# Optimization experiments

Measured on AMD Instinct MI355X. Metric: run time of the kernel, lower is better.

## Reference

```python
import jax, jax.numpy as jnp
import numpy as np
from jax.scipy.special import logsumexp

N_NODES = 10000
DEG = 16            # fixed out-degree -> 1-hop neighborhood size m = DEG + 1
N_TPL = 16
TPL_N = 10
N_FEAT = 128
N_SINK = 10         # Sinkhorn iterations for the linear OT subproblem
N_CG = 4            # Frank-Wolfe (conditional gradient) iterations for FGW


def setup_inputs() -> dict:
    key = jax.random.key(0)
    k1, k2, k3 = jax.random.split(key, 3)
    x = jax.random.normal(k1, (N_NODES, N_FEAT), jnp.float32)
    # structured fixed-degree graph: node i -> (i+1..i+DEG) mod N, sorted by source
    src = jnp.repeat(jnp.arange(N_NODES), DEG)
    dst = ((jnp.arange(N_NODES)[:, None] + jnp.arange(1, DEG + 1)[None, :]) % N_NODES).reshape(-1)
    edge_index = jnp.stack([src, dst])
    R = jax.random.uniform(k2, (N_TPL, TPL_N, TPL_N), jnp.float32)
    templates = 0.5 * (R + jnp.swapaxes(R, 1, 2))           # symmetric, as in template_initialisation
    templates_features = 0.001 * jax.random.normal(k3, (N_TPL, TPL_N, N_FEAT), jnp.float32)
    q0 = jnp.zeros((N_TPL, TPL_N), jnp.float32)
    alpha0 = jnp.zeros((1,), jnp.float32)
    return {"x": x, "templates": templates, "templates_features": templates_features,
            "q0": q0, "alpha0": alpha0, "edge_index": edge_index}


def _sinkhorn_log(G, logp, logq, reg):
    """Entropic OT plan for cost G [m,n], marginals exp(logp), exp(logq); log-domain."""
    def body(carry, _):
        f, g = carry
        f = reg * logp - reg * logsumexp((g[None, :] - G) / reg, axis=1)
        g = reg * logq - reg * logsumexp((f[:, None] - G) / reg, axis=0)
        return (f, g), None
    (f, g), _ = jax.lax.scan(jax.checkpoint(body),
                             (jnp.zeros_like(logp), jnp.zeros_like(logq)), None, length=N_SINK)
    return jnp.exp((f[:, None] + g[None, :] - G) / reg)


def _fgw(C1, F1, p, C2, F2, q, alpha):
    """Fused GW distance (square loss) between (C1 [m,m], F1 [m,d], p [m]) and
    (C2 [n,n], F2 [n,d], q [n]) via conditional gradient with Sinkhorn LP solver."""
    # squared-euclidean feature cost  [m,n]
    M = jnp.sum(F1 * F1, 1)[:, None] + jnp.sum(F2 * F2, 1)[None, :] - 2.0 * (F1 @ F2.T)
    # constant term of the square-loss GW tensor product
    constC = ((C1 * C1) @ p)[:, None] + ((C2 * C2) @ q)[None, :]
    logp, logq = jnp.log(p), jnp.log(q)
    T0 = p[:, None] * q[None, :]

    def cg(T, _):
        CTC = C1 @ T @ C2                                   # [m,n]
        Gr = (1.0 - alpha) * M + 2.0 * alpha * (constC - 2.0 * CTC)   # FGW gradient
        reg = 0.01 * jnp.max(jnp.abs(Gr)) + 1e-8            # small entropic reg ~ EMD
        Tn = _sinkhorn_log(Gr, logp, logq, reg)
        D = Tn - T
        CDC = C1 @ D @ C2
        # E(T + t D) is quadratic in t:  a t^2 + b t + const
        a = -2.0 * alpha * jnp.sum(CDC * D)
        b = (1.0 - alpha) * jnp.sum(M * D) + alpha * (jnp.sum(constC * D) - 4.0 * jnp.sum(CTC * D))
        t = jnp.where(a > 0, jnp.clip(-b / (2.0 * a + 1e-16), 0.0, 1.0),
                      jnp.where(a + b < 0, 1.0, 0.0))
        return T + t * D, None

    T, _ = jax.lax.scan(jax.checkpoint(cg), T0, None, length=N_CG)
    return (1.0 - alpha) * jnp.sum(M * T) + alpha * jnp.sum((constC - 2.0 * C1 @ T @ C2) * T)


def reference(x, templates, templates_features, q0, alpha0, edge_index):
    N, d = x.shape
    deg = edge_index.shape[1] // N
    m = deg + 1
    neighbors = edge_index[1].reshape(N, deg)                       # sorted-by-source
    local = jnp.concatenate([jnp.arange(N)[:, None], neighbors], 1)  # [N,m] node + 1-hop
    # local adjacency: edge (a,b) iff local[b] in neighbors(local[a]); symmetrized
    neigh_loc = neighbors[local]                                    # [N,m,deg]
    C1 = (neigh_loc[:, :, None, :] == local[:, None, :, None]).any(-1).astype(x.dtype)
    C1 = jnp.maximum(C1, jnp.swapaxes(C1, 1, 2))                    # [N,m,m]
    F1 = x[local]                                                   # [N,m,d]
    alpha = jax.nn.sigmoid(alpha0[0])
    q = jax.nn.softmax(q0, axis=1)                                  # [K,n]
    p = jnp.full((m,), 1.0 / m, x.dtype)
    over_tpl = jax.vmap(_fgw, in_axes=(None, None, None, 0, 0, 0, None))
    over_nodes = jax.vmap(over_tpl, in_axes=(0, 0, None, None, None, None, None))
    dist = over_nodes(C1, F1, p, templates, templates_features, q, alpha)  # [N,K]
    return jnp.log(dist)
```

## Files before the change

kernel.cpp:

```cpp
#include <hip/hip_runtime.h>
#include <math.h>

#define NN    10000
#define MM    17
#define KT    16
#define TN    10
#define NH    5
#define NF    128
#define NSINK 10
#define NCG   4
#define DOTLD (NN*TN)

typedef float v2f __attribute__((ext_vector_type(2)));
__device__ __forceinline__ v2f mk2(float x, float y) { v2f r; r.x = x; r.y = y; return r; }

#define ELEM(arr, b2) (((b2) & 1) ? arr[(b2) >> 1].y : arr[(b2) >> 1].x)

template <int CTRL>
__device__ __forceinline__ float dppf(float v) {
    return __int_as_float(__builtin_amdgcn_update_dpp(
        0, __float_as_int(v), CTRL, 0xF, 0xF, true));
}
__device__ __forceinline__ float rsum4(float v) {
    v += dppf<0xB1>(v);
    v += dppf<0x4E>(v);
    return v;
}
__device__ __forceinline__ float rmax4(float v) {
    v = fmaxf(v, dppf<0xB1>(v));
    v = fmaxf(v, dppf<0x4E>(v));
    return v;
}

__device__ __forceinline__ float dot4(float4 a, float4 b) {
    return a.x*b.x + a.y*b.y + a.z*b.z + a.w*b.w;
}

__global__ __launch_bounds__(256)
void precompute_kernel(const float* __restrict__ x, const float* __restrict__ tfeat,
                       float* __restrict__ dot_t, float* __restrict__ xnorm,
                       float* __restrict__ tfnorm)
{
    __shared__ float4 tfs[TN * (NF / 4)];
    __shared__ float4 xs[256 * 4];

    const int k   = blockIdx.y;
    const int v0  = blockIdx.x * 256;
    const int tid = threadIdx.x;
    const int v   = v0 + tid;
    const int vc  = (v < NN) ? v : (NN - 1);

    const float4* tf4 = (const float4*)(tfeat + (size_t)k * TN * NF);
    for (int u = tid; u < TN * (NF / 4); u += 256) tfs[u] = tf4[u];
    __syncthreads();

    if (blockIdx.x == 0 && tid < TN) {
        float s = 0.f;
        #pragma unroll 8
        for (int c = 0; c < NF / 4; ++c) { float4 u = tfs[tid * (NF / 4) + c]; s += dot4(u, u); }
        tfnorm[k * TN + tid] = s;
    }

    float acc[TN];
    #pragma unroll
    for (int j = 0; j < TN; ++j) acc[j] = 0.f;
    float xa = 0.f;

    const float4* x4 = (const float4*)x;
    for (int ch = 0; ch < 8; ++ch) {
        __syncthreads();
        for (int u = tid; u < 256 * 4; u += 256) {
            int vr = u >> 2, c4 = u & 3;
            int vv = v0 + vr; if (vv >= NN) vv = NN - 1;
            xs[u] = x4[(size_t)vv * (NF / 4) + ch * 4 + c4];
        }
        __syncthreads();
        float4 xv0 = xs[tid * 4 + 0], xv1 = xs[tid * 4 + 1],
               xv2 = xs[tid * 4 + 2], xv3 = xs[tid * 4 + 3];
        xa += dot4(xv0, xv0) + dot4(xv1, xv1) + dot4(xv2, xv2) + dot4(xv3, xv3);
        #pragma unroll
        for (int j = 0; j < TN; ++j) {
            const float4* tr = &tfs[j * (NF / 4) + ch * 4];
            acc[j] += dot4(xv0, tr[0]) + dot4(xv1, tr[1])
                    + dot4(xv2, tr[2]) + dot4(xv3, tr[3]);
        }
    }

    if (v < NN) {
        float* dst = dot_t + (size_t)k * DOTLD + (size_t)vc * TN;
        #pragma unroll
        for (int j = 0; j < NH; ++j) {
            *(v2f*)(dst + 2 * j) = mk2(acc[2 * j], acc[2 * j + 1]);
        }
        if (k == 0) xnorm[vc] = xa;
    }
}

__global__ __launch_bounds__(256, 2)
void fgw_main(const float* __restrict__ dot_t,
              const float* __restrict__ xnorm,
              const float* __restrict__ tfnorm,
              const float* __restrict__ templates,
              const float* __restrict__ q0,
              const float* __restrict__ alpha0,
              float* __restrict__ out)
{
    const int k    = blockIdx.y;
    const int tid  = threadIdx.x;
    const int l    = tid & 3;
    const int node = blockIdx.x * 64 + (tid >> 2);

    const float* __restrict__ C2  = templates + k * (TN * TN);
    const float* __restrict__ q0r = q0 + k * TN;
    const float* __restrict__ tfn = tfnorm + k * TN;
    const float* __restrict__ dk  = dot_t + (size_t)k * DOTLD;

    const float alpha = 1.0f / (1.0f + __expf(-alpha0[0]));
    const float oma   = 1.0f - alpha;
    const float t2a   = 2.0f * alpha;

    float qs_[TN];
    float qmax = q0r[0];
    #pragma unroll
    for (int b = 1; b < TN; ++b) qmax = fmaxf(qmax, q0r[b]);
    float qsum = 0.f;
    #pragma unroll
    for (int b = 0; b < TN; ++b) { qs_[b] = __expf(q0r[b] - qmax); qsum += qs_[b]; }
    float inv_qs = 1.0f / qsum;
    v2f qv2[NH];
    #pragma unroll
    for (int j = 0; j < NH; ++j) qv2[j] = mk2(qs_[2*j] * inv_qs, qs_[2*j+1] * inv_qs);

    v2f accc[NH], base[NH];
    #pragma unroll
    for (int j = 0; j < NH; ++j) { accc[j] = mk2(0.f, 0.f); base[j] = mk2(0.f, 0.f); }
    #pragma unroll
    for (int b2 = 0; b2 < TN; ++b2) {
        float qb2 = ELEM(qv2, b2);
        #pragma unroll
        for (int j = 0; j < NH; ++j) {
            v2f cr = mk2(C2[(2*j) * TN + b2], C2[(2*j+1) * TN + b2]);
            v2f cc = *(const v2f*)(C2 + b2 * TN + 2*j);
            accc[j] += (cr * cr) * qb2;
            base[j] += qb2 * cc;
        }
    }
    #pragma unroll
    for (int j = 0; j < NH; ++j) {
        accc[j] = alpha * (accc[j] + (float)(MM - 1) / (float)MM);
        base[j] = 2.0f * accc[j] - (4.0f * alpha * (float)(MM - 1) / (float)MM) * base[j];
    }

    int v1 = node + l;      if (v1 >= NN) v1 -= NN;
    int v2 = node + l + 4;  if (v2 >= NN) v2 -= NN;
    int v3 = node + l + 8;  if (v3 >= NN) v3 -= NN;
    int v4 = node + l + 12; if (v4 >= NN) v4 -= NN;
    int vB = node + 16;     if (vB >= NN) vB -= NN;
    const float ox1 = oma * xnorm[v1], ox2 = oma * xnorm[v2], ox3 = oma * xnorm[v3],
                ox4 = oma * xnorm[v4], oxB = oma * xnorm[vB];
    const float m2o = -2.0f * oma;
    const float* __restrict__ d1 = dk + (size_t)v1 * TN;
    const float* __restrict__ d2 = dk + (size_t)v2 * TN;
    const float* __restrict__ d3 = dk + (size_t)v3 * TN;
    const float* __restrict__ d4 = dk + (size_t)v4 * TN;
    const float* __restrict__ dB = dk + (size_t)vB * TN;

    v2f Gr1[NH], Gr2[NH], Gr3[NH], Gr4[NH], GrB[NH];
    #pragma unroll
    for (int j = 0; j < NH; ++j) {
        v2f bt = base[j] + oma * mk2(tfn[2*j], tfn[2*j+1]);
        Gr1[j] = (bt + ox1) + m2o * (*(const v2f*)(d1 + 2*j));
        Gr2[j] = (bt + ox2) + m2o * (*(const v2f*)(d2 + 2*j));
        Gr3[j] = (bt + ox3) + m2o * (*(const v2f*)(d3 + 2*j));
        Gr4[j] = (bt + ox4) + m2o * (*(const v2f*)(d4 + 2*j));
        GrB[j] = (bt + oxB) + m2o * (*(const v2f*)(dB + 2*j));
    }

    v2f T1[NH], T2[NH], T3[NH], T4[NH], TB[NH];
    #pragma unroll
    for (int j = 0; j < NH; ++j) {
        v2f t0 = (1.0f / (float)MM) * qv2[j];
        T1[j] = t0; T2[j] = t0; T3[j] = t0; T4[j] = t0; TB[j] = t0;
    }

    for (int cg = 0; cg < NCG; ++cg) {
        float gm = 0.f;
        #pragma unroll
        for (int j = 0; j < NH; ++j) {
            gm = fmaxf(gm, fmaxf(fabsf(Gr1[j].x), fabsf(Gr1[j].y)));
            gm = fmaxf(gm, fmaxf(fabsf(Gr2[j].x), fabsf(Gr2[j].y)));
            gm = fmaxf(gm, fmaxf(fabsf(Gr3[j].x), fabsf(Gr3[j].y)));
            gm = fmaxf(gm, fmaxf(fabsf(Gr4[j].x), fabsf(Gr4[j].y)));
            gm = fmaxf(gm, fmaxf(fabsf(GrB[j].x), fabsf(GrB[j].y)));
        }
        gm = rmax4(gm);
        const float reg = 0.01f * gm + 1e-8f;
        const float invreg = 1.0f / reg;

        float r1 = fminf(Gr1[0].x, Gr1[0].y), r2 = fminf(Gr2[0].x, Gr2[0].y);
        float r3 = fminf(Gr3[0].x, Gr3[0].y), r4 = fminf(Gr4[0].x, Gr4[0].y);
        float rB = fminf(GrB[0].x, GrB[0].y);
        #pragma unroll
        for (int j = 1; j < NH; ++j) {
            r1 = fminf(r1, fminf(Gr1[j].x, Gr1[j].y));
            r2 = fminf(r2, fminf(Gr2[j].x, Gr2[j].y));
            r3 = fminf(r3, fminf(Gr3[j].x, Gr3[j].y));
            r4 = fminf(r4, fminf(Gr4[j].x, Gr4[j].y));
            rB = fminf(rB, fminf(GrB[j].x, GrB[j].y));
        }
        v2f E1[NH], E2[NH], E3[NH], E4[NH], EB[NH];
        #pragma unroll
        for (int j = 0; j < NH; ++j) {
            v2f a1 = (r1 - Gr1[j]) * invreg; E1[j] = mk2(__expf(a1.x), __expf(a1.y));
            v2f a2 = (r2 - Gr2[j]) * invreg; E2[j] = mk2(__expf(a2.x), __expf(a2.y));
            v2f a3 = (r3 - Gr3[j]) * invreg; E3[j] = mk2(__expf(a3.x), __expf(a3.y));
            v2f a4 = (r4 - Gr4[j]) * invreg; E4[j] = mk2(__expf(a4.x), __expf(a4.y));
            v2f aB = (rB - GrB[j]) * invreg; EB[j] = mk2(__expf(aB.x), __expf(aB.y));
        }

        v2f egp[NH];
        #pragma unroll
        for (int j = 0; j < NH; ++j) egp[j] = mk2(1.f, 1.f);
        float w1 = 0.f, w2 = 0.f, w3 = 0.f, w4 = 0.f, wB = 0.f;
        for (int it = 0; it < NSINK; ++it) {
            v2f a1 = mk2(0.f,0.f), a2 = mk2(0.f,0.f), a3 = mk2(0.f,0.f),
                a4 = mk2(0.f,0.f), aB = mk2(0.f,0.f);
            #pragma unroll
            for (int j = 0; j < NH; ++j) {
                a1 += egp[j] * E1[j]; a2 += egp[j] * E2[j]; a3 += egp[j] * E3[j];
                a4 += egp[j] * E4[j]; aB += egp[j] * EB[j];
            }
            w1 = __builtin_amdgcn_rcpf(a1.x + a1.y);
            w2 = __builtin_amdgcn_rcpf(a2.x + a2.y);
            w3 = __builtin_amdgcn_rcpf(a3.x + a3.y);
            w4 = __builtin_amdgcn_rcpf(a4.x + a4.y);
            wB = __builtin_amdgcn_rcpf(aB.x + aB.y);
            #pragma unroll
            for (int j = 0; j < NH; ++j) {
                v2f t = w1 * E1[j] + w2 * E2[j] + w3 * E3[j] + w4 * E4[j];
                float Sx = fmaf(wB, EB[j].x, rsum4(t.x));
                float Sy = fmaf(wB, EB[j].y, rsum4(t.y));
                egp[j] = qv2[j] * mk2(__builtin_amdgcn_rcpf(Sx), __builtin_amdgcn_rcpf(Sy));
            }
        }

        v2f D1[NH], D2[NH], D3[NH], D4[NH], DB[NH];
        #pragma unroll
        for (int j = 0; j < NH; ++j) {
            D1[j] = (w1 * egp[j]) * E1[j] - T1[j];
            D2[j] = (w2 * egp[j]) * E2[j] - T2[j];
            D3[j] = (w3 * egp[j]) * E3[j] - T3[j];
            D4[j] = (w4 * egp[j]) * E4[j] - T4[j];
            DB[j] = (wB * egp[j]) * EB[j] - TB[j];
        }
        v2f cs[NH];
        #pragma unroll
        for (int j = 0; j < NH; ++j) {
            v2f dp = D1[j] + D2[j] + D3[j] + D4[j];
            cs[j] = mk2(rsum4(dp.x), rsum4(dp.y)) + DB[j];
        }
        v2f cdc1[NH], cdc2[NH], cdc3[NH], cdc4[NH], cdcB[NH];
        #pragma unroll
        for (int j = 0; j < NH; ++j) {
            cdc1[j] = mk2(0.f,0.f); cdc2[j] = mk2(0.f,0.f); cdc3[j] = mk2(0.f,0.f);
            cdc4[j] = mk2(0.f,0.f); cdcB[j] = mk2(0.f,0.f);
        }
        #pragma unroll
        for (int b2 = 0; b2 < TN; ++b2) {
            float csb = ELEM(cs, b2);
            float u1 = csb - ELEM(D1, b2), u2 = csb - ELEM(D2, b2),
                  u3 = csb - ELEM(D3, b2), u4 = csb - ELEM(D4, b2),
                  uB = csb - ELEM(DB, b2);
            #pragma unroll
            for (int j = 0; j < NH; ++j) {
                v2f c = *(const v2f*)(C2 + b2 * TN + 2*j);
                cdc1[j] += u1 * c; cdc2[j] += u2 * c; cdc3[j] += u3 * c;
                cdc4[j] += u4 * c; cdcB[j] += uB * c;
            }
        }
        v2f pAv = mk2(0.f,0.f), pBv = mk2(0.f,0.f), pAB = mk2(0.f,0.f), pBB = mk2(0.f,0.f);
        #pragma unroll
        for (int j = 0; j < NH; ++j) {
            pAv += cdc1[j] * D1[j] + cdc2[j] * D2[j] + cdc3[j] * D3[j] + cdc4[j] * D4[j];
            pAB += cdcB[j] * DB[j];
            pBv += (Gr1[j] - accc[j]) * D1[j] + (Gr2[j] - accc[j]) * D2[j]
                 + (Gr3[j] - accc[j]) * D3[j] + (Gr4[j] - accc[j]) * D4[j];
            pBB += (GrB[j] - accc[j]) * DB[j];
        }
        float pA = rsum4(pAv.x + pAv.y) + (pAB.x + pAB.y);
        float pB = rsum4(pBv.x + pBv.y) + (pBB.x + pBB.y);
        float ac = -t2a * pA;
        float bc = pB;
        float t;
        if (ac > 0.f) { t = -bc / (2.0f * ac + 1e-16f); t = fminf(fmaxf(t, 0.f), 1.f); }
        else          { t = (ac + bc < 0.f) ? 1.0f : 0.0f; }
        const float gc = -2.0f * t2a * t;
        #pragma unroll
        for (int j = 0; j < NH; ++j) {
            T1[j] += t * D1[j]; T2[j] += t * D2[j]; T3[j] += t * D3[j];
            T4[j] += t * D4[j]; TB[j] += t * DB[j];
            Gr1[j] += gc * cdc1[j]; Gr2[j] += gc * cdc2[j]; Gr3[j] += gc * cdc3[j];
            Gr4[j] += gc * cdc4[j]; GrB[j] += gc * cdcB[j];
        }
    }

    v2f cs[NH];
    #pragma unroll
    for (int j = 0; j < NH; ++j) {
        v2f tp = T1[j] + T2[j] + T3[j] + T4[j];
        cs[j] = mk2(rsum4(tp.x), rsum4(tp.y)) + TB[j];
    }
    v2f pFv = mk2(0.f,0.f), pFB = mk2(0.f,0.f);
    #pragma unroll
    for (int j = 0; j < NH; ++j) {
        v2f ct1 = mk2(0.f,0.f), ct2 = mk2(0.f,0.f), ct3 = mk2(0.f,0.f),
            ct4 = mk2(0.f,0.f), ctB = mk2(0.f,0.f);
        #pragma unroll
        for (int b2 = 0; b2 < TN; ++b2) {
            float csb = ELEM(cs, b2);
            v2f c = *(const v2f*)(C2 + b2 * TN + 2*j);
            ct1 += (csb - ELEM(T1, b2)) * c;
            ct2 += (csb - ELEM(T2, b2)) * c;
            ct3 += (csb - ELEM(T3, b2)) * c;
            ct4 += (csb - ELEM(T4, b2)) * c;
            ctB += (csb - ELEM(TB, b2)) * c;
        }
        pFv += (Gr1[j] - accc[j] + t2a * ct1) * T1[j]
             + (Gr2[j] - accc[j] + t2a * ct2) * T2[j]
             + (Gr3[j] - accc[j] + t2a * ct3) * T3[j]
             + (Gr4[j] - accc[j] + t2a * ct4) * T4[j];
        pFB += (GrB[j] - accc[j] + t2a * ctB) * TB[j];
    }
    float pF = rsum4(pFv.x + pFv.y) + (pFB.x + pFB.y);
    if (l == 0 && node < NN) out[node * KT + k] = logf(pF);
}

extern "C" void kernel_launch(void* const* d_in, const int* in_sizes, int n_in,
                              void* d_out, int out_size, void* d_ws, size_t ws_size,
                              hipStream_t stream)
{
    const float* x         = (const float*)d_in[0];
    const float* templates = (const float*)d_in[1];
    const float* tfeat     = (const float*)d_in[2];
    const float* q0        = (const float*)d_in[3];
    const float* alpha0    = (const float*)d_in[4];

    float* dot_t  = (float*)d_ws;
    float* xnorm  = dot_t + (size_t)KT * DOTLD;
    float* tfnorm = xnorm + NN;

    dim3 pgrid((NN + 255) / 256, KT);
    precompute_kernel<<<pgrid, 256, 0, stream>>>(x, tfeat, dot_t, xnorm, tfnorm);

    dim3 grid((NN + 63) / 64, KT);
    fgw_main<<<grid, 256, 0, stream>>>(dot_t, xnorm, tfnorm, templates, q0, alpha0, (float*)d_out);
}
```

Measured before the change: 192.5 us.

## Track FGW objective incrementally and hoist per-template constants into precompute

```diff
diff --git a/kernel.cpp b/kernel.cpp
--- a/kernel.cpp
+++ b/kernel.cpp
@@ -10,6 +10,7 @@
 #define NSINK 10
 #define NCG   4
 #define DOTLD (NN*TN)
+#define KCW   32
 
 typedef float v2f __attribute__((ext_vector_type(2)));
 __device__ __forceinline__ v2f mk2(float x, float y) { v2f r; r.x = x; r.y = y; return r; }
@@ -38,11 +39,14 @@
 
 __global__ __launch_bounds__(256)
 void precompute_kernel(const float* __restrict__ x, const float* __restrict__ tfeat,
+                       const float* __restrict__ templates,
+                       const float* __restrict__ q0, const float* __restrict__ alpha0,
                        float* __restrict__ dot_t, float* __restrict__ xnorm,
-                       float* __restrict__ tfnorm)
+                       float* __restrict__ kcst)
 {
     __shared__ float4 tfs[TN * (NF / 4)];
     __shared__ float4 xs[256 * 4];
+    __shared__ float  tns[TN];
 
     const int k   = blockIdx.y;
     const int v0  = blockIdx.x * 256;
@@ -58,7 +62,41 @@
         float s = 0.f;
         #pragma unroll 8
         for (int c = 0; c < NF / 4; ++c) { float4 u = tfs[tid * (NF / 4) + c]; s += dot4(u, u); }
-        tfnorm[k * TN + tid] = s;
+        tns[tid] = s;
+    }
+    __syncthreads();
+
+    if (blockIdx.x == 0 && tid == 0) {
+        const float* C2 = templates + k * (TN * TN);
+        const float alpha = 1.0f / (1.0f + __expf(-alpha0[0]));
+        const float oma = 1.0f - alpha;
+        float qv[TN];
+        float qmax = q0[k * TN];
+        for (int b = 1; b < TN; ++b) qmax = fmaxf(qmax, q0[k * TN + b]);
+        float qs = 0.f;
+        for (int b = 0; b < TN; ++b) { qv[b] = __expf(q0[k * TN + b] - qmax); qs += qv[b]; }
+        float inv = 1.0f / qs;
+        for (int b = 0; b < TN; ++b) qv[b] *= inv;
+        float* kc = kcst + k * KCW;
+        const float c1pp = (float)(MM - 1) / (float)MM;
+        float fc = 0.f;
+        for (int b = 0; b < TN; ++b) {
+            float cc = 0.f, qc = 0.f;
+            for (int b2 = 0; b2 < TN; ++b2) {
+                float cb = C2[b * TN + b2];
+                cc += cb * cb * qv[b2];
+                qc += C2[b2 * TN + b] * qv[b2];
+            }
+            float accc = alpha * (c1pp + cc);
+            float ctc0 = c1pp * qc;
+            float bt   = 2.0f * accc - 4.0f * alpha * ctc0 + oma * tns[b];
+            kc[b]      = qv[b];
+            kc[10 + b] = accc;
+            kc[20 + b] = bt;
+            fc += qv[b] * (2.0f * alpha * ctc0 - accc);
+        }
+        kc[30] = fc;
+        kc[31] = alpha;
     }
 
     float acc[TN];
@@ -96,59 +134,32 @@
     }
 }
 
-__global__ __launch_bounds__(256, 2)
+__global__ __launch_bounds__(64, 4)
 void fgw_main(const float* __restrict__ dot_t,
               const float* __restrict__ xnorm,
-              const float* __restrict__ tfnorm,
-              const float* __restrict__ templates,
-              const float* __restrict__ q0,
+              const float* __restrict__ kcst,
               const float* __restrict__ alpha0,
               float* __restrict__ out)
 {
     const int k    = blockIdx.y;
     const int tid  = threadIdx.x;
     const int l    = tid & 3;
-    const int node = blockIdx.x * 64 + (tid >> 2);
-
-    const float* __restrict__ C2  = templates + k * (TN * TN);
-    const float* __restrict__ q0r = q0 + k * TN;
-    const float* __restrict__ tfn = tfnorm + k * TN;
-    const float* __restrict__ dk  = dot_t + (size_t)k * DOTLD;
-
-    const float alpha = 1.0f / (1.0f + __expf(-alpha0[0]));
+    const int node = blockIdx.x * 16 + (tid >> 2);
+
+    const float* __restrict__ kc = kcst + k * KCW;
+    const float* __restrict__ dk = dot_t + (size_t)k * DOTLD;
+
+    const float alpha = kc[31];
     const float oma   = 1.0f - alpha;
     const float t2a   = 2.0f * alpha;
-
-    float qs_[TN];
-    float qmax = q0r[0];
-    #pragma unroll
-    for (int b = 1; b < TN; ++b) qmax = fmaxf(qmax, q0r[b]);
-    float qsum = 0.f;
-    #pragma unroll
-    for (int b = 0; b < TN; ++b) { qs_[b] = __expf(q0r[b] - qmax); qsum += qs_[b]; }
-    float inv_qs = 1.0f / qsum;
-    v2f qv2[NH];
-    #pragma unroll
-    for (int j = 0; j < NH; ++j) qv2[j] = mk2(qs_[2*j] * inv_qs, qs_[2*j+1] * inv_qs);
-
-    v2f accc[NH], base[NH];
-    #pragma unroll
-    for (int j = 0; j < NH; ++j) { accc[j] = mk2(0.f, 0.f); base[j] = mk2(0.f, 0.f); }
-    #pragma unroll
-    for (int b2 = 0; b2 < TN; ++b2) {
-        float qb2 = ELEM(qv2, b2);
-        #pragma unroll
-        for (int j = 0; j < NH; ++j) {
-            v2f cr = mk2(C2[(2*j) * TN + b2], C2[(2*j+1) * TN + b2]);
-            v2f cc = *(const v2f*)(C2 + b2 * TN + 2*j);
-            accc[j] += (cr * cr) * qb2;
-            base[j] += qb2 * cc;
-        }
-    }
+    const float fc    = kc[30];
+
+    v2f qv2[NH], accc[NH], bt[NH];
     #pragma unroll
     for (int j = 0; j < NH; ++j) {
-        accc[j] = alpha * (accc[j] + (float)(MM - 1) / (float)MM);
-        base[j] = 2.0f * accc[j] - (4.0f * alpha * (float)(MM - 1) / (float)MM) * base[j];
+        qv2[j]  = mk2(kc[2*j],      kc[2*j+1]);
+        accc[j] = mk2(kc[10 + 2*j], kc[10 + 2*j+1]);
+        bt[j]   = mk2(kc[20 + 2*j], kc[20 + 2*j+1]);
     }
 
     int v1 = node + l;      if (v1 >= NN) v1 -= NN;
@@ -168,13 +179,21 @@
     v2f Gr1[NH], Gr2[NH], Gr3[NH], Gr4[NH], GrB[NH];
     #pragma unroll
     for (int j = 0; j < NH; ++j) {
-        v2f bt = base[j] + oma * mk2(tfn[2*j], tfn[2*j+1]);
-        Gr1[j] = (bt + ox1) + m2o * (*(const v2f*)(d1 + 2*j));
-        Gr2[j] = (bt + ox2) + m2o * (*(const v2f*)(d2 + 2*j));
-        Gr3[j] = (bt + ox3) + m2o * (*(const v2f*)(d3 + 2*j));
-        Gr4[j] = (bt + ox4) + m2o * (*(const v2f*)(d4 + 2*j));
-        GrB[j] = (bt + oxB) + m2o * (*(const v2f*)(dB + 2*j));
-    }
+        Gr1[j] = (bt[j] + ox1) + m2o * (*(const v2f*)(d1 + 2*j));
+        Gr2[j] = (bt[j] + ox2) + m2o * (*(const v2f*)(d2 + 2*j));
+        Gr3[j] = (bt[j] + ox3) + m2o * (*(const v2f*)(d3 + 2*j));
+        Gr4[j] = (bt[j] + ox4) + m2o * (*(const v2f*)(d4 + 2*j));
+        GrB[j] = (bt[j] + oxB) + m2o * (*(const v2f*)(dB + 2*j));
+    }
+
+    v2f fA = mk2(0.f, 0.f), fB = mk2(0.f, 0.f);
+    #pragma unroll
+    for (int j = 0; j < NH; ++j) {
+        v2f g4 = Gr1[j] + Gr2[j] + Gr3[j] + Gr4[j];
+        fA += qv2[j] * g4;
+        fB += qv2[j] * GrB[j];
+    }
+    float F = (rsum4(fA.x + fA.y) + (fB.x + fB.y)) * (1.0f / (float)MM) + fc;
 
     v2f T1[NH], T2[NH], T3[NH], T4[NH], TB[NH];
     #pragma unroll
@@ -183,6 +202,7 @@
         T1[j] = t0; T2[j] = t0; T3[j] = t0; T4[j] = t0; TB[j] = t0;
     }
 
+    #pragma unroll
     for (int cg = 0; cg < NCG; ++cg) {
         float gm = 0.f;
         #pragma unroll
@@ -259,6 +279,7 @@
             v2f dp = D1[j] + D2[j] + D3[j] + D4[j];
             cs[j] = mk2(rsum4(dp.x), rsum4(dp.y)) + DB[j];
         }
+        const float* __restrict__ C2 = kcst + KT * KCW + k * (TN * TN);
         v2f cdc1[NH], cdc2[NH], cdc3[NH], cdc4[NH], cdcB[NH];
         #pragma unroll
         for (int j = 0; j < NH; ++j) {
@@ -294,45 +315,20 @@
         float t;
         if (ac > 0.f) { t = -bc / (2.0f * ac + 1e-16f); t = fminf(fmaxf(t, 0.f), 1.f); }
         else          { t = (ac + bc < 0.f) ? 1.0f : 0.0f; }
-        const float gc = -2.0f * t2a * t;
-        #pragma unroll
-        for (int j = 0; j < NH; ++j) {
-            T1[j] += t * D1[j]; T2[j] += t * D2[j]; T3[j] += t * D3[j];
-            T4[j] += t * D4[j]; TB[j] += t * DB[j];
-            Gr1[j] += gc * cdc1[j]; Gr2[j] += gc * cdc2[j]; Gr3[j] += gc * cdc3[j];
-            Gr4[j] += gc * cdc4[j]; GrB[j] += gc * cdcB[j];
-        }
-    }
-
-    v2f cs[NH];
-    #pragma unroll
-    for (int j = 0; j < NH; ++j) {
-        v2f tp = T1[j] + T2[j] + T3[j] + T4[j];
-        cs[j] = mk2(rsum4(tp.x), rsum4(tp.y)) + TB[j];
-    }
-    v2f pFv = mk2(0.f,0.f), pFB = mk2(0.f,0.f);
-    #pragma unroll
-    for (int j = 0; j < NH; ++j) {
-        v2f ct1 = mk2(0.f,0.f), ct2 = mk2(0.f,0.f), ct3 = mk2(0.f,0.f),
-            ct4 = mk2(0.f,0.f), ctB = mk2(0.f,0.f);
-        #pragma unroll
-        for (int b2 = 0; b2 < TN; ++b2) {
-            float csb = ELEM(cs, b2);
-            v2f c = *(const v2f*)(C2 + b2 * TN + 2*j);
-            ct1 += (csb - ELEM(T1, b2)) * c;
-            ct2 += (csb - ELEM(T2, b2)) * c;
-            ct3 += (csb - ELEM(T3, b2)) * c;
-            ct4 += (csb - ELEM(T4, b2)) * c;
-            ctB += (csb - ELEM(TB, b2)) * c;
-        }
-        pFv += (Gr1[j] - accc[j] + t2a * ct1) * T1[j]
-             + (Gr2[j] - accc[j] + t2a * ct2) * T2[j]
-             + (Gr3[j] - accc[j] + t2a * ct3) * T3[j]
-             + (Gr4[j] - accc[j] + t2a * ct4) * T4[j];
-        pFB += (GrB[j] - accc[j] + t2a * ctB) * TB[j];
-    }
-    float pF = rsum4(pFv.x + pFv.y) + (pFB.x + pFB.y);
-    if (l == 0 && node < NN) out[node * KT + k] = logf(pF);
+        F = fmaf(t, fmaf(t, ac, bc), F);
+        if (cg != NCG - 1) {
+            const float gc = -2.0f * t2a * t;
+            #pragma unroll
+            for (int j = 0; j < NH; ++j) {
+                T1[j] += t * D1[j]; T2[j] += t * D2[j]; T3[j] += t * D3[j];
+                T4[j] += t * D4[j]; TB[j] += t * DB[j];
+                Gr1[j] += gc * cdc1[j]; Gr2[j] += gc * cdc2[j]; Gr3[j] += gc * cdc3[j];
+                Gr4[j] += gc * cdc4[j]; GrB[j] += gc * cdcB[j];
+            }
+        }
+    }
+
+    if (l == 0) out[node * KT + k] = logf(F);
 }
 
 extern "C" void kernel_launch(void* const* d_in, const int* in_sizes, int n_in,
@@ -347,11 +343,16 @@
 
     float* dot_t  = (float*)d_ws;
     float* xnorm  = dot_t + (size_t)KT * DOTLD;
-    float* tfnorm = xnorm + NN;
+    float* kcst   = xnorm + NN;
+    float* tplcpy = kcst + KT * KCW;
+
+    hipMemcpyAsync(tplcpy, templates, (size_t)KT * TN * TN * sizeof(float),
+                   hipMemcpyDeviceToDevice, stream);
 
     dim3 pgrid((NN + 255) / 256, KT);
-    precompute_kernel<<<pgrid, 256, 0, stream>>>(x, tfeat, dot_t, xnorm, tfnorm);
-
-    dim3 grid((NN + 63) / 64, KT);
-    fgw_main<<<grid, 256, 0, stream>>>(dot_t, xnorm, tfnorm, templates, q0, alpha0, (float*)d_out);
-}
+    precompute_kernel<<<pgrid, 256, 0, stream>>>(x, tfeat, templates, q0, alpha0,
+                                                 dot_t, xnorm, kcst);
+
+    dim3 grid(NN / 16, KT);
+    fgw_main<<<grid, 64, 0, stream>>>(dot_t, xnorm, kcst, alpha0, (float*)d_out);
+}
```

New measurement: 388.7 us. 2.02x slower.
